# Kernel optimization log

Measured on AMD Instinct MI355X. Metric: run time of the kernel, lower is better.

## Reference

```python
import jax, jax.numpy as jnp
import numpy as np

HEADS = 8
DIM_HEAD = 64
WINDOW = 8  # local_window_size


def _sn_weight(W, u, sigma):
    """SNLinear reparameterized weight: one power-iteration step (detached)
    then sigma_W = v^T W u (grad flows through W only), weight = W/sigma_W * sigma."""
    v = W @ u
    v = v / jnp.linalg.norm(v)
    u2 = W.T @ v
    u2 = u2 / jnp.linalg.norm(u2)
    v = jax.lax.stop_gradient(v)
    u2 = jax.lax.stop_gradient(u2)
    sigma_w = jnp.einsum('c,cd,d->', v, W, u2)
    return W / sigma_w * sigma


def setup_inputs() -> dict:
    key = jax.random.key(0)
    ks = jax.random.split(key, 6)
    B, S, D = 2, 2048, 512
    inner = HEADS * DIM_HEAD  # 512
    x = jax.random.normal(ks[0], (B, S, D), dtype=jnp.float32)
    W_qkv = 0.02 * jax.random.normal(ks[1], (3 * inner, D), dtype=jnp.float32)
    u_qkv = jax.random.normal(ks[2], (D,), dtype=jnp.float32)
    u_qkv = u_qkv / jnp.linalg.norm(u_qkv)
    W_out = 0.02 * jax.random.normal(ks[3], (D, inner), dtype=jnp.float32)
    b_out = jnp.zeros((D,), dtype=jnp.float32)
    u_out = jax.random.normal(ks[4], (inner,), dtype=jnp.float32)
    u_out = u_out / jnp.linalg.norm(u_out)
    sigma_qkv = jnp.ones((1,), dtype=jnp.float32)
    sigma_out = jnp.ones((1,), dtype=jnp.float32)
    temperature = jnp.asarray(np.log(DIM_HEAD ** -0.5), dtype=jnp.float32)
    return {
        'x': x, 'W_qkv': W_qkv, 'u_qkv': u_qkv, 'sigma_qkv': sigma_qkv,
        'W_out': W_out, 'b_out': b_out, 'u_out': u_out, 'sigma_out': sigma_out,
        'temperature': temperature,
    }


def reference(x, W_qkv, u_qkv, sigma_qkv, W_out, b_out, u_out, sigma_out, temperature):
    B, S, D = x.shape
    # qkv projection (spectral-normed, no bias)
    Wq = _sn_weight(W_qkv, u_qkv, sigma_qkv[0])
    qkv = x @ Wq.T                                   # [B,S,3*inner]
    q, k, v = jnp.split(qkv, 3, axis=-1)
    to_heads = lambda t: t.reshape(B, S, HEADS, DIM_HEAD).transpose(0, 2, 1, 3)
    q, k, v = to_heads(q), to_heads(k), to_heads(v)   # [B,H,S,Dh]
    dots = jnp.einsum('bhid,bhjd->bhij', q, k) * jnp.exp(temperature)
    # local causal band mask (True inside band); original masked_fill fills True
    i = jnp.arange(S)
    band = (i[:, None] >= i[None, :]) & ((i[:, None] - i[None, :]) <= (WINDOW - 1))
    neg = -jnp.finfo(dots.dtype).max
    dots = jnp.where(band[None, None, :, :], neg, dots)
    attn = jax.nn.softmax(dots, axis=-1)
    out = jnp.einsum('bhij,bhjd->bhid', attn, v)      # [B,H,S,Dh]
    out = out.transpose(0, 2, 1, 3).reshape(B, S, HEADS * DIM_HEAD)
    Wo = _sn_weight(W_out, u_out, sigma_out[0])
    return out @ Wo.T + b_out
```

## Files before the change

### kernel.cpp

```cpp
#include <hip/hip_runtime.h>
#include <hip/hip_bf16.h>
#include <math.h>

#define HEADS 8
#define DH 64
#define SEQ 2048
#define BATCH 2
#define DMODEL 512
#define INNER 512
#define WIN 8

typedef unsigned short ushort_t;
typedef __attribute__((ext_vector_type(8))) __bf16 bf16x8;
typedef __attribute__((ext_vector_type(8))) unsigned short u16x8;
typedef __attribute__((ext_vector_type(4))) float f32x4;

__device__ inline float bf2f(ushort_t u) {
    unsigned v = ((unsigned)u) << 16; float f; __builtin_memcpy(&f, &v, 4); return f;
}
__device__ inline ushort_t f2bf(float f) {
    __hip_bfloat16 h = __float2bfloat16(f); ushort_t u; __builtin_memcpy(&u, &h, 2); return u;
}
__device__ inline float fast_exp2(float x) { return __builtin_amdgcn_exp2f(x); }
__device__ inline int swz_idx(int row, int col) { return ((row << 6) | col) ^ ((row & 7) << 3); }

__device__ inline bf16x8 ld_frag(const ushort_t* lds, int row, int col) {
    u16x8 v = *(const u16x8*)&lds[swz_idx(row, col)];
    return __builtin_bit_cast(bf16x8, v);
}
__device__ inline f32x4 mfma16(bf16x8 a, bf16x8 b, f32x4 c) {
    return __builtin_amdgcn_mfma_f32_16x16x32_bf16(a, b, c, 0, 0, 0);
}
__device__ inline void gload16(const void* g, void* l) {
    __builtin_amdgcn_global_load_lds(
        (const __attribute__((address_space(1))) unsigned int*)g,
        (__attribute__((address_space(3))) unsigned int*)l, 16, 0, 0);
}

__global__ __launch_bounds__(256) void fused_cast_sn1(const float* __restrict__ x,
                                                      const float* __restrict__ Wq,
                                                      const float* __restrict__ Wo,
                                                      const float* __restrict__ uq,
                                                      const float* __restrict__ uo,
                                                      ushort_t* __restrict__ xb,
                                                      ushort_t* __restrict__ wqb,
                                                      ushort_t* __restrict__ wob,
                                                      float* __restrict__ zbuf,
                                                      float* __restrict__ v1,
                                                      float* __restrict__ v2) {
    const int b = blockIdx.x;
    if (b < 1536) {
        const int gid = b * 256 + threadIdx.x;
        const float* src; ushort_t* dst; int g;
        if (gid < 262144)      { src = x;  dst = xb;  g = gid; }
        else if (gid < 360448) { src = Wq; dst = wqb; g = gid - 262144; }
        else                   { src = Wo; dst = wob; g = gid - 360448; }
        float4 a = *(const float4*)&src[(size_t)g * 8];
        float4 c = *(const float4*)&src[(size_t)g * 8 + 4];
        u16x8 o;
        o[0] = f2bf(a.x); o[1] = f2bf(a.y); o[2] = f2bf(a.z); o[3] = f2bf(a.w);
        o[4] = f2bf(c.x); o[5] = f2bf(c.y); o[6] = f2bf(c.z); o[7] = f2bf(c.w);
        *(u16x8*)&dst[(size_t)g * 8] = o;
        if (gid < 1032) zbuf[gid] = 0.f;
    } else {
        const int lane = threadIdx.x & 63, w = threadIdx.x >> 6;
        const int r = (b - 1536) * 4 + w;
        const float* W; const float* u; float* vout; int rr;
        if (r < 1536) { W = Wq; u = uq; vout = v1; rr = r; }
        else          { W = Wo; u = uo; vout = v2; rr = r - 1536; }
        float4 w0 = *(const float4*)&W[(size_t)rr * 512 + lane * 8];
        float4 w1 = *(const float4*)&W[(size_t)rr * 512 + lane * 8 + 4];
        float4 u0 = *(const float4*)&u[lane * 8];
        float4 u1 = *(const float4*)&u[lane * 8 + 4];
        float dot = w0.x * u0.x + w0.y * u0.y + w0.z * u0.z + w0.w * u0.w +
                    w1.x * u1.x + w1.y * u1.y + w1.z * u1.z + w1.w * u1.w;
#pragma unroll
        for (int off = 1; off < 64; off <<= 1) dot += __shfl_xor(dot, off, 64);
        if (lane == 0) vout[rr] = dot;
    }
}

__global__ __launch_bounds__(256) void fused_sn2_sn3(const float* __restrict__ Wq,
                                                     const float* __restrict__ Wo,
                                                     const float* __restrict__ v1,
                                                     const float* __restrict__ v2,
                                                     float* __restrict__ z1,
                                                     float* __restrict__ z2,
                                                     float* __restrict__ counter,
                                                     const float* __restrict__ sq,
                                                     const float* __restrict__ so,
                                                     float* __restrict__ scales) {
    __shared__ float red[256];
    __shared__ int is_last;
    const int t = threadIdx.x, b = blockIdx.x;
    {
        const float* W; const float* v; float* z; int r0;
        if (b < 96) { W = Wq; v = v1; z = z1; r0 = b * 16; }
        else        { W = Wo; v = v2; z = z2; r0 = (b - 96) * 16; }
        float a0 = 0.f, a1 = 0.f;
        for (int i = 0; i < 16; ++i) {
            float vv = v[r0 + i];
            a0 += W[(size_t)(r0 + i) * 512 + t] * vv;
            a1 += W[(size_t)(r0 + i) * 512 + 256 + t] * vv;
        }
        atomicAdd(&z[t], a0);
        atomicAdd(&z[t + 256], a1);
    }
    __threadfence();
    __syncthreads();
    if (t == 0) is_last = (atomicAdd(counter, 1.0f) == 127.0f);
    __syncthreads();
    if (!is_last) return;
    __threadfence();
    for (int which = 0; which < 2; ++which) {
        const float* v = which ? v2 : v1;
        const float* z = which ? z2 : z1;
        const int R = which ? 512 : 1536;
        float n1 = 0.f;
        for (int i = t; i < R; i += 256) { float q = v[i]; n1 += q * q; }
        red[t] = n1; __syncthreads();
        for (int off = 128; off > 0; off >>= 1) { if (t < off) red[t] += red[t + off]; __syncthreads(); }
        n1 = red[0]; __syncthreads();
        float n2 = 0.f;
        for (int i = t; i < 512; i += 256) { float q = z[i]; n2 += q * q; }
        red[t] = n2; __syncthreads();
        for (int off = 128; off > 0; off >>= 1) { if (t < off) red[t] += red[t + off]; __syncthreads(); }
        if (t == 0) scales[which] = (which ? so[0] : sq[0]) * sqrtf(n1 / red[0]);
        __syncthreads();
    }
}

__global__ __launch_bounds__(256) void gemm_bt_qkv(const ushort_t* __restrict__ A,
                                                   const ushort_t* __restrict__ B,
                                                   ushort_t* __restrict__ qkv) {
    constexpr int K = DMODEL;
    __shared__ ushort_t As[8 * 128 * 8];
    __shared__ ushort_t Bs[8 * 64 * 8];
    const int t = threadIdx.x, lane = t & 63, w = t >> 6;
    const int wm = w >> 1, wn = w & 1, lg = lane >> 4, li = lane & 15;
    const int m0 = blockIdx.y * 128, n0 = blockIdx.x * 64;
    f32x4 acc[4][2] = {};
    for (int k0 = 0; k0 < K; k0 += 64) {
        __syncthreads();
#pragma unroll
        for (int i = 0; i < 4; ++i) {
            int j = w * 4 + i;
            int kc = j >> 1, mh = (j & 1) * 64;
            gload16(&A[(size_t)(m0 + mh + lane) * K + k0 + kc * 8], &As[(kc * 128 + mh) * 8]);
        }
#pragma unroll
        for (int i = 0; i < 2; ++i) {
            int kc = w * 2 + i;
            gload16(&B[(size_t)(n0 + lane) * K + k0 + kc * 8], &Bs[(kc * 64) * 8]);
        }
        __syncthreads();
#pragma unroll
        for (int kw = 0; kw < 2; ++kw) {
            bf16x8 af[4], bf[2];
#pragma unroll
            for (int mi = 0; mi < 4; ++mi)
                af[mi] = *(const bf16x8*)&As[((kw * 4 + lg) * 128 + wm * 64 + mi * 16 + li) * 8];
#pragma unroll
            for (int ni = 0; ni < 2; ++ni)
                bf[ni] = *(const bf16x8*)&Bs[((kw * 4 + lg) * 64 + wn * 32 + ni * 16 + li) * 8];
#pragma unroll
            for (int mi = 0; mi < 4; ++mi)
#pragma unroll
                for (int ni = 0; ni < 2; ++ni)
                    acc[mi][ni] = mfma16(af[mi], bf[ni], acc[mi][ni]);
        }
    }
    ushort_t* vT = qkv + (size_t)2 * BATCH * HEADS * SEQ * DH;
    if (n0 >= 1024) {
#pragma unroll
        for (int mi = 0; mi < 4; ++mi) {
            int base = m0 + wm * 64 + mi * 16 + lg * 4;
            int bb = base >> 11, ss = base & 2047;
#pragma unroll
            for (int ni = 0; ni < 2; ++ni) {
                int n = n0 + wn * 32 + ni * 16 + li;
                int h = (n >> 6) & 7, d0 = n & 63;
                ushort4 o;
                o.x = f2bf(acc[mi][ni][0]); o.y = f2bf(acc[mi][ni][1]);
                o.z = f2bf(acc[mi][ni][2]); o.w = f2bf(acc[mi][ni][3]);
                *(ushort4*)&vT[((size_t)((bb * HEADS + h) * DH) + d0) * SEQ + ss] = o;
            }
        }
    } else {
#pragma unroll
        for (int mi = 0; mi < 4; ++mi)
#pragma unroll
            for (int r = 0; r < 4; ++r) {
                int row = m0 + wm * 64 + mi * 16 + lg * 4 + r;
                int bb = row >> 11, ss = row & 2047;
#pragma unroll
                for (int ni = 0; ni < 2; ++ni) {
                    int n = n0 + wn * 32 + ni * 16 + li;
                    int which = n >> 9, h = (n >> 6) & 7, d0 = n & 63;
                    qkv[(size_t)which * (BATCH * HEADS * SEQ * DH) +
                        ((size_t)((bb * HEADS + h) * SEQ) + ss) * DH + d0] = f2bf(acc[mi][ni][r]);
                }
            }
    }
}

__global__ __launch_bounds__(256) void gemm_bt_out(const ushort_t* __restrict__ A,
                                                   const ushort_t* __restrict__ B,
                                                   const float* __restrict__ scales,
                                                   const float* __restrict__ bias,
                                                   float* __restrict__ C) {
    constexpr int K = INNER;
    __shared__ ushort_t As[8 * 64 * 8];
    __shared__ ushort_t Bs[8 * 64 * 8];
    const int t = threadIdx.x, lane = t & 63, w = t >> 6;
    const int wm = w >> 1, wn = w & 1, lg = lane >> 4, li = lane & 15;
    const int m0 = blockIdx.y * 64, n0 = blockIdx.x * 64;
    f32x4 acc[2][2] = {};
    for (int k0 = 0; k0 < K; k0 += 64) {
        __syncthreads();
#pragma unroll
        for (int i = 0; i < 2; ++i) {
            int kc = w * 2 + i;
            gload16(&A[(size_t)(m0 + lane) * K + k0 + kc * 8], &As[(kc * 64) * 8]);
            gload16(&B[(size_t)(n0 + lane) * K + k0 + kc * 8], &Bs[(kc * 64) * 8]);
        }
        __syncthreads();
#pragma unroll
        for (int kw = 0; kw < 2; ++kw) {
            bf16x8 af[2], bf[2];
#pragma unroll
            for (int mi = 0; mi < 2; ++mi)
                af[mi] = *(const bf16x8*)&As[((kw * 4 + lg) * 64 + wm * 32 + mi * 16 + li) * 8];
#pragma unroll
            for (int ni = 0; ni < 2; ++ni)
                bf[ni] = *(const bf16x8*)&Bs[((kw * 4 + lg) * 64 + wn * 32 + ni * 16 + li) * 8];
#pragma unroll
            for (int mi = 0; mi < 2; ++mi)
#pragma unroll
                for (int ni = 0; ni < 2; ++ni)
                    acc[mi][ni] = mfma16(af[mi], bf[ni], acc[mi][ni]);
        }
    }
    const float sc = scales[0] * scales[1];
#pragma unroll
    for (int mi = 0; mi < 2; ++mi)
#pragma unroll
        for (int r = 0; r < 4; ++r) {
            int row = m0 + wm * 32 + mi * 16 + lg * 4 + r;
#pragma unroll
            for (int ni = 0; ni < 2; ++ni) {
                int n = n0 + wn * 32 + ni * 16 + li;
                C[(size_t)row * INNER + n] = acc[mi][ni][r] * sc + bias[n];
            }
        }
}

__global__ __launch_bounds__(512) void attn_mfma_kernel(const ushort_t* __restrict__ qkv,
                                                        const float* __restrict__ temp,
                                                        const float* __restrict__ scales,
                                                        ushort_t* __restrict__ attn_out) {
    __shared__ ushort_t kvbuf[2 * 4 * 4096];
    __shared__ ushort_t Pl[2 * 4096];
    const int t    = threadIdx.x;
    const int lane = t & 63, w = t >> 6;
    const int g    = w >> 2, wl = w & 3;
    const int lg   = lane >> 4, li = lane & 15;
    const int bh   = blockIdx.x >> 5;
    const int i0   = (blockIdx.x & 31) * 64;
    const ushort_t* qp  = qkv;
    const ushort_t* kp  = qkv + (size_t)BATCH * HEADS * SEQ * DH;
    const ushort_t* vTp = kp  + (size_t)BATCH * HEADS * SEQ * DH;
    const ushort_t* kp_bh  = kp  + (size_t)bh * SEQ * DH;
    const ushort_t* vTp_bh = vTp + (size_t)bh * DH * SEQ;
    const float s0 = scales[0];
    const float st = expf(temp[0]) * s0 * s0 * 1.44269504088896340736f;

    ushort_t* Pb = Pl + g * 4096;
    const int srw = lane >> 3;
    const int sc  = (lane & 7) ^ srw;

    bf16x8 aQ[2];
#pragma unroll
    for (int c = 0; c < 2; ++c) {
        u16x8 qv = *(const u16x8*)&qp[((size_t)bh * SEQ + i0 + 16 * wl + li) * DH + 32 * c + lg * 8];
        u16x8 r;
#pragma unroll
        for (int j = 0; j < 8; ++j) r[j] = f2bf(bf2f(qv[j]) * st);
        aQ[c] = __builtin_bit_cast(bf16x8, r);
    }

    float lsum[4] = {0.f, 0.f, 0.f, 0.f};
    f32x4 oacc[4] = {};

    auto STAGE = [&](int jtn, int tbuf) {
#pragma unroll
        for (int i = 0; i < 4; ++i) {
            const int sid = i * 8 + w;
            const int bsel = sid >> 3;
            const int srow8 = sid & 7;
            const int row = srow8 * 8 + srw;
            const ushort_t* gsrc;
            if (bsel < 2)
                gsrc = kp_bh + (size_t)(jtn * 128 + bsel * 64 + row) * DH + sc * 8;
            else
                gsrc = vTp_bh + (size_t)row * SEQ + jtn * 128 + (bsel - 2) * 64 + sc * 8;
            gload16(gsrc, &kvbuf[tbuf * 16384 + bsel * 4096 + srow8 * 512]);
        }
    };

    STAGE(0, 0);
    __syncthreads();

    int cur = 0;
    for (int jt = 0; jt < SEQ / 128; ++jt) {
        if (jt < SEQ / 128 - 1) STAGE(jt + 1, cur ^ 1);
        const ushort_t* Kb = kvbuf + cur * 16384 + g * 4096;
        const ushort_t* Vb = kvbuf + cur * 16384 + 8192 + g * 4096;
        const int j0 = jt * 128 + g * 64;

        f32x4 s[4];
        __builtin_amdgcn_s_setprio(1);
#pragma unroll
        for (int kc = 0; kc < 4; ++kc) {
            bf16x8 b0 = ld_frag(Kb, kc * 16 + li, lg * 8);
            bf16x8 b1 = ld_frag(Kb, kc * 16 + li, 32 + lg * 8);
            f32x4 z = {0.f, 0.f, 0.f, 0.f};
            z = mfma16(aQ[0], b0, z);
            z = mfma16(aQ[1], b1, z);
            s[kc] = z;
        }
        __builtin_amdgcn_s_setprio(0);
        const bool need_mask = (j0 == i0) || (j0 == i0 - 64);
        if (need_mask) {
#pragma unroll
            for (int kc = 0; kc < 4; ++kc)
#pragma unroll
                for (int r = 0; r < 4; ++r) {
                    int qi = i0 + 16 * wl + lg * 4 + r;
                    int kj = j0 + kc * 16 + li;
                    float pv = ((unsigned)(qi - kj) < (unsigned)WIN) ? 0.f : fast_exp2(s[kc][r]);
                    lsum[r] += pv;
                    Pb[swz_idx(16 * wl + lg * 4 + r, kc * 16 + li)] = f2bf(pv);
                }
        } else {
#pragma unroll
            for (int kc = 0; kc < 4; ++kc)
#pragma unroll
                for (int r = 0; r < 4; ++r) {
                    float pv = fast_exp2(s[kc][r]);
                    lsum[r] += pv;
                    Pb[swz_idx(16 * wl + lg * 4 + r, kc * 16 + li)] = f2bf(pv);
                }
        }
        bf16x8 aP[2];
#pragma unroll
        for (int c = 0; c < 2; ++c) aP[c] = ld_frag(Pb, 16 * wl + li, c * 32 + lg * 8);
        __builtin_amdgcn_s_setprio(1);
#pragma unroll
        for (int tt = 0; tt < 4; ++tt) {
            bf16x8 b0 = ld_frag(Vb, tt * 16 + li, lg * 8);
            bf16x8 b1 = ld_frag(Vb, tt * 16 + li, 32 + lg * 8);
            oacc[tt] = mfma16(aP[0], b0, oacc[tt]);
            oacc[tt] = mfma16(aP[1], b1, oacc[tt]);
        }
        __builtin_amdgcn_s_setprio(0);
        __syncthreads();
        cur ^= 1;
    }

#pragma unroll
    for (int r = 0; r < 4; ++r) {
        float l = lsum[r];
        l += __shfl_xor(l, 1, 16);
        l += __shfl_xor(l, 2, 16);
        l += __shfl_xor(l, 4, 16);
        l += __shfl_xor(l, 8, 16);
        lsum[r] = l;
    }
    float* O_part = (float*)kvbuf;
    float* lsr    = (float*)Pl;
    if (g == 1) {
#pragma unroll
        for (int r = 0; r < 4; ++r) {
            int row = 16 * wl + lg * 4 + r;
            if (li == 0) lsr[row] = lsum[r];
#pragma unroll
            for (int tt = 0; tt < 4; ++tt)
                O_part[row * 68 + tt * 16 + li] = oacc[tt][r];
        }
    }
    __syncthreads();
    if (g == 0) {
        const int b_ = bh >> 3, h = bh & 7;
#pragma unroll
        for (int r = 0; r < 4; ++r) {
            int row = 16 * wl + lg * 4 + r;
            float inv = 1.0f / (lsum[r] + lsr[row]);
            size_t base = ((size_t)(b_ * SEQ + i0 + row)) * INNER + h * DH;
#pragma unroll
            for (int tt = 0; tt < 4; ++tt)
                attn_out[base + tt * 16 + li] =
                    f2bf((oacc[tt][r] + O_part[row * 68 + tt * 16 + li]) * inv);
        }
    }
}

extern "C" void kernel_launch(void* const* d_in, const int* in_sizes, int n_in,
                              void* d_out, int out_size, void* d_ws, size_t ws_size,
                              hipStream_t stream) {
    const float* x     = (const float*)d_in[0];
    const float* W_qkv = (const float*)d_in[1];
    const float* u_qkv = (const float*)d_in[2];
    const float* s_qkv = (const float*)d_in[3];
    const float* W_out = (const float*)d_in[4];
    const float* b_out = (const float*)d_in[5];
    const float* u_out = (const float*)d_in[6];
    const float* s_out = (const float*)d_in[7];
    const float* temp  = (const float*)d_in[8];
    float* out = (float*)d_out;

    float* scales  = (float*)d_ws;
    float* v1      = scales + 64;
    float* v2      = v1 + 1536;
    float* z1      = v2 + 512;
    float* z2      = z1 + 512;
    float* counter = z1 + 1024;
    ushort_t* xb    = (ushort_t*)((char*)d_ws + 16384);
    ushort_t* wqb   = xb + (size_t)2097152;
    ushort_t* wob   = wqb + (size_t)786432;
    ushort_t* qkvb  = wob + (size_t)262144;
    ushort_t* attnb = qkvb + (size_t)6291456;

    fused_cast_sn1<<<dim3(2048), dim3(256), 0, stream>>>(x, W_qkv, W_out, u_qkv, u_out,
                                                         xb, wqb, wob, z1, v1, v2);
    fused_sn2_sn3<<<dim3(128), dim3(256), 0, stream>>>(W_qkv, W_out, v1, v2, z1, z2,
                                                       counter, s_qkv, s_out, scales);
    gemm_bt_qkv<<<dim3(24, 32), dim3(256), 0, stream>>>(xb, wqb, qkvb);
    attn_mfma_kernel<<<dim3(512), dim3(512), 0, stream>>>(qkvb, temp, scales, attnb);
    gemm_bt_out<<<dim3(8, 64), dim3(256), 0, stream>>>(attnb, wob, scales, b_out, out);
}
```

Baseline: 160.9 us.

## Merge spectral-norm reduction into QKV GEMM launch and transpose score MFMA layout

The separate spectral-norm second-stage kernel becomes extra blocks appended to the QKV GEMM grid, which is flattened to 1D, removing one kernel launch and letting the small reduction overlap with GEMM tiles. In the attention kernel the score MFMA operands are swapped, so each lane holds four consecutive key columns for a single query row. The P tile is then written with a vectorized ushort4 store, and the row-sum collapses to one scalar per lane that needs only two cross-lane shuffles. The denominators from both key halves are exchanged through shared memory. A risk is that the scale-producing blocks must finish before the attention kernel reads the scales, which still holds because of stream ordering.

```diff
diff --git a/kernel.cpp b/kernel.cpp
--- a/kernel.cpp
+++ b/kernel.cpp
@@ -80,65 +80,69 @@
     }
 }
 
-__global__ __launch_bounds__(256) void fused_sn2_sn3(const float* __restrict__ Wq,
-                                                     const float* __restrict__ Wo,
-                                                     const float* __restrict__ v1,
-                                                     const float* __restrict__ v2,
-                                                     float* __restrict__ z1,
-                                                     float* __restrict__ z2,
-                                                     float* __restrict__ counter,
-                                                     const float* __restrict__ sq,
-                                                     const float* __restrict__ so,
-                                                     float* __restrict__ scales) {
-    __shared__ float red[256];
-    __shared__ int is_last;
-    const int t = threadIdx.x, b = blockIdx.x;
-    {
-        const float* W; const float* v; float* z; int r0;
-        if (b < 96) { W = Wq; v = v1; z = z1; r0 = b * 16; }
-        else        { W = Wo; v = v2; z = z2; r0 = (b - 96) * 16; }
-        float a0 = 0.f, a1 = 0.f;
-        for (int i = 0; i < 16; ++i) {
-            float vv = v[r0 + i];
-            a0 += W[(size_t)(r0 + i) * 512 + t] * vv;
-            a1 += W[(size_t)(r0 + i) * 512 + 256 + t] * vv;
-        }
-        atomicAdd(&z[t], a0);
-        atomicAdd(&z[t + 256], a1);
-    }
-    __threadfence();
-    __syncthreads();
-    if (t == 0) is_last = (atomicAdd(counter, 1.0f) == 127.0f);
-    __syncthreads();
-    if (!is_last) return;
-    __threadfence();
-    for (int which = 0; which < 2; ++which) {
-        const float* v = which ? v2 : v1;
-        const float* z = which ? z2 : z1;
-        const int R = which ? 512 : 1536;
-        float n1 = 0.f;
-        for (int i = t; i < R; i += 256) { float q = v[i]; n1 += q * q; }
-        red[t] = n1; __syncthreads();
-        for (int off = 128; off > 0; off >>= 1) { if (t < off) red[t] += red[t + off]; __syncthreads(); }
-        n1 = red[0]; __syncthreads();
-        float n2 = 0.f;
-        for (int i = t; i < 512; i += 256) { float q = z[i]; n2 += q * q; }
-        red[t] = n2; __syncthreads();
-        for (int off = 128; off > 0; off >>= 1) { if (t < off) red[t] += red[t + off]; __syncthreads(); }
-        if (t == 0) scales[which] = (which ? so[0] : sq[0]) * sqrtf(n1 / red[0]);
-        __syncthreads();
-    }
-}
-
-__global__ __launch_bounds__(256) void gemm_bt_qkv(const ushort_t* __restrict__ A,
+__global__ __launch_bounds__(256) void gemm_qkv_sn(const ushort_t* __restrict__ A,
                                                    const ushort_t* __restrict__ B,
-                                                   ushort_t* __restrict__ qkv) {
+                                                   ushort_t* __restrict__ qkv,
+                                                   const float* __restrict__ Wq,
+                                                   const float* __restrict__ Wo,
+                                                   const float* __restrict__ v1,
+                                                   const float* __restrict__ v2,
+                                                   float* __restrict__ z1,
+                                                   float* __restrict__ z2,
+                                                   float* __restrict__ counter,
+                                                   const float* __restrict__ sq,
+                                                   const float* __restrict__ so,
+                                                   float* __restrict__ scales) {
     constexpr int K = DMODEL;
     __shared__ ushort_t As[8 * 128 * 8];
     __shared__ ushort_t Bs[8 * 64 * 8];
-    const int t = threadIdx.x, lane = t & 63, w = t >> 6;
+    __shared__ float red[256];
+    __shared__ int is_last;
+    const int t = threadIdx.x;
+
+    if (blockIdx.x >= 768) {
+        const int b = blockIdx.x - 768;
+        {
+            const float* W; const float* v; float* z; int r0;
+            if (b < 96) { W = Wq; v = v1; z = z1; r0 = b * 16; }
+            else        { W = Wo; v = v2; z = z2; r0 = (b - 96) * 16; }
+            float a0 = 0.f, a1 = 0.f;
+            for (int i = 0; i < 16; ++i) {
+                float vv = v[r0 + i];
+                a0 += W[(size_t)(r0 + i) * 512 + t] * vv;
+                a1 += W[(size_t)(r0 + i) * 512 + 256 + t] * vv;
+            }
+            atomicAdd(&z[t], a0);
+            atomicAdd(&z[t + 256], a1);
+        }
+        __threadfence();
+        __syncthreads();
+        if (t == 0) is_last = (atomicAdd(counter, 1.0f) == 127.0f);
+        __syncthreads();
+        if (!is_last) return;
+        __threadfence();
+        for (int which = 0; which < 2; ++which) {
+            const float* v = which ? v2 : v1;
+            const float* z = which ? z2 : z1;
+            const int R = which ? 512 : 1536;
+            float n1 = 0.f;
+            for (int i = t; i < R; i += 256) { float q = v[i]; n1 += q * q; }
+            red[t] = n1; __syncthreads();
+            for (int off = 128; off > 0; off >>= 1) { if (t < off) red[t] += red[t + off]; __syncthreads(); }
+            n1 = red[0]; __syncthreads();
+            float n2 = 0.f;
+            for (int i = t; i < 512; i += 256) { float q = z[i]; n2 += q * q; }
+            red[t] = n2; __syncthreads();
+            for (int off = 128; off > 0; off >>= 1) { if (t < off) red[t] += red[t + off]; __syncthreads(); }
+            if (t == 0) scales[which] = (which ? so[0] : sq[0]) * sqrtf(n1 / red[0]);
+            __syncthreads();
+        }
+        return;
+    }
+
+    const int lane = t & 63, w = t >> 6;
     const int wm = w >> 1, wn = w & 1, lg = lane >> 4, li = lane & 15;
-    const int m0 = blockIdx.y * 128, n0 = blockIdx.x * 64;
+    const int m0 = (blockIdx.x / 24) * 128, n0 = (blockIdx.x % 24) * 64;
     f32x4 acc[4][2] = {};
     for (int k0 = 0; k0 < K; k0 += 64) {
         __syncthreads();
@@ -289,8 +293,9 @@
         aQ[c] = __builtin_bit_cast(bf16x8, r);
     }
 
-    float lsum[4] = {0.f, 0.f, 0.f, 0.f};
+    float lsum = 0.f;
     f32x4 oacc[4] = {};
+    const int qi = i0 + 16 * wl + li;
 
     auto STAGE = [&](int jtn, int tbuf) {
 #pragma unroll
@@ -325,32 +330,29 @@
             bf16x8 b0 = ld_frag(Kb, kc * 16 + li, lg * 8);
             bf16x8 b1 = ld_frag(Kb, kc * 16 + li, 32 + lg * 8);
             f32x4 z = {0.f, 0.f, 0.f, 0.f};
-            z = mfma16(aQ[0], b0, z);
-            z = mfma16(aQ[1], b1, z);
+            z = mfma16(b0, aQ[0], z);
+            z = mfma16(b1, aQ[1], z);
             s[kc] = z;
         }
         __builtin_amdgcn_s_setprio(0);
         const bool need_mask = (j0 == i0) || (j0 == i0 - 64);
-        if (need_mask) {
-#pragma unroll
-            for (int kc = 0; kc < 4; ++kc)
-#pragma unroll
-                for (int r = 0; r < 4; ++r) {
-                    int qi = i0 + 16 * wl + lg * 4 + r;
-                    int kj = j0 + kc * 16 + li;
-                    float pv = ((unsigned)(qi - kj) < (unsigned)WIN) ? 0.f : fast_exp2(s[kc][r]);
-                    lsum[r] += pv;
-                    Pb[swz_idx(16 * wl + lg * 4 + r, kc * 16 + li)] = f2bf(pv);
-                }
-        } else {
-#pragma unroll
-            for (int kc = 0; kc < 4; ++kc)
-#pragma unroll
-                for (int r = 0; r < 4; ++r) {
-                    float pv = fast_exp2(s[kc][r]);
-                    lsum[r] += pv;
-                    Pb[swz_idx(16 * wl + lg * 4 + r, kc * 16 + li)] = f2bf(pv);
-                }
+#pragma unroll
+        for (int kc = 0; kc < 4; ++kc) {
+            float p0, p1, p2, p3;
+            if (need_mask) {
+                int kjb = j0 + kc * 16 + lg * 4;
+                p0 = ((unsigned)(qi - kjb - 0) < (unsigned)WIN) ? 0.f : fast_exp2(s[kc][0]);
+                p1 = ((unsigned)(qi - kjb - 1) < (unsigned)WIN) ? 0.f : fast_exp2(s[kc][1]);
+                p2 = ((unsigned)(qi - kjb - 2) < (unsigned)WIN) ? 0.f : fast_exp2(s[kc][2]);
+                p3 = ((unsigned)(qi - kjb - 3) < (unsigned)WIN) ? 0.f : fast_exp2(s[kc][3]);
+            } else {
+                p0 = fast_exp2(s[kc][0]); p1 = fast_exp2(s[kc][1]);
+                p2 = fast_exp2(s[kc][2]); p3 = fast_exp2(s[kc][3]);
+            }
+            lsum += (p0 + p1) + (p2 + p3);
+            ushort4 o;
+            o.x = f2bf(p0); o.y = f2bf(p1); o.z = f2bf(p2); o.w = f2bf(p3);
+            *(ushort4*)&Pb[swz_idx(16 * wl + li, kc * 16 + lg * 4)] = o;
         }
         bf16x8 aP[2];
 #pragma unroll
@@ -368,22 +370,15 @@
         cur ^= 1;
     }
 
-#pragma unroll
-    for (int r = 0; r < 4; ++r) {
-        float l = lsum[r];
-        l += __shfl_xor(l, 1, 16);
-        l += __shfl_xor(l, 2, 16);
-        l += __shfl_xor(l, 4, 16);
-        l += __shfl_xor(l, 8, 16);
-        lsum[r] = l;
-    }
+    lsum += __shfl_xor(lsum, 16, 64);
+    lsum += __shfl_xor(lsum, 32, 64);
+    float* den    = (float*)Pl;
     float* O_part = (float*)kvbuf;
-    float* lsr    = (float*)Pl;
+    if (lg == 0) den[g * 64 + 16 * wl + li] = lsum;
     if (g == 1) {
 #pragma unroll
         for (int r = 0; r < 4; ++r) {
             int row = 16 * wl + lg * 4 + r;
-            if (li == 0) lsr[row] = lsum[r];
 #pragma unroll
             for (int tt = 0; tt < 4; ++tt)
                 O_part[row * 68 + tt * 16 + li] = oacc[tt][r];
@@ -395,7 +390,7 @@
 #pragma unroll
         for (int r = 0; r < 4; ++r) {
             int row = 16 * wl + lg * 4 + r;
-            float inv = 1.0f / (lsum[r] + lsr[row]);
+            float inv = 1.0f / (den[row] + den[64 + row]);
             size_t base = ((size_t)(b_ * SEQ + i0 + row)) * INNER + h * DH;
 #pragma unroll
             for (int tt = 0; tt < 4; ++tt)
@@ -433,9 +428,8 @@
 
     fused_cast_sn1<<<dim3(2048), dim3(256), 0, stream>>>(x, W_qkv, W_out, u_qkv, u_out,
                                                          xb, wqb, wob, z1, v1, v2);
-    fused_sn2_sn3<<<dim3(128), dim3(256), 0, stream>>>(W_qkv, W_out, v1, v2, z1, z2,
-                                                       counter, s_qkv, s_out, scales);
-    gemm_bt_qkv<<<dim3(24, 32), dim3(256), 0, stream>>>(xb, wqb, qkvb);
+    gemm_qkv_sn<<<dim3(896), dim3(256), 0, stream>>>(xb, wqb, qkvb, W_qkv, W_out, v1, v2,
+                                                     z1, z2, counter, s_qkv, s_out, scales);
     attn_mfma_kernel<<<dim3(512), dim3(512), 0, stream>>>(qkvb, temp, scales, attnb);
     gemm_bt_out<<<dim3(8, 64), dim3(256), 0, stream>>>(attnb, wob, scales, b_out, out);
 }
```

After: 164.1 us. 2.0% more time.
